# Kernel tuning notes

Hardware: AMD Instinct MI355X
Metric: run time of the kernel (lower is better)

The kernel has to match this reference:

```python
import jax, jax.numpy as jnp
from jax import lax
import numpy as np

DELTA = 2
KUP = 5


def setup_inputs() -> dict:
    key = jax.random.key(0)
    ks = jax.random.split(key, 7)
    N, C, H, W = 4, 256, 64, 64
    Cm, outC = 64, 256
    enc_out = DELTA ** 2 * KUP ** 2  # 100
    return {
        "x": jax.random.normal(ks[0], (N, C, H, W), dtype=jnp.float32),
        "W_down": jax.random.normal(ks[1], (Cm, C), dtype=jnp.float32) * (1.0 / np.sqrt(C)),
        "b_down": jax.random.normal(ks[2], (Cm,), dtype=jnp.float32) * 0.01,
        "W_enc": jax.random.normal(ks[3], (enc_out, Cm, 3, 3), dtype=jnp.float32) * (1.0 / np.sqrt(Cm * 9)),
        "b_enc": jax.random.normal(ks[4], (enc_out,), dtype=jnp.float32) * 0.01,
        "W_out": jax.random.normal(ks[5], (outC, C), dtype=jnp.float32) * (1.0 / np.sqrt(C)),
        "b_out": jax.random.normal(ks[6], (outC,), dtype=jnp.float32) * 0.01,
    }


def reference(x, W_down, b_down, W_enc, b_enc, W_out, b_out):
    N, C, H, W = x.shape
    d, Kup = DELTA, KUP
    K2, d2 = Kup * Kup, d * d

    # 1x1 down conv (Cm channels)
    t = jnp.einsum('nchw,mc->nmhw', x, W_down) + b_down[None, :, None, None]
    # 3x3 encoder conv -> (N, K2*d2, H, W); channel layout (k, i, j) as in torch pixel_shuffle
    e = lax.conv_general_dilated(t, W_enc, (1, 1), 'SAME',
                                 dimension_numbers=('NCHW', 'OIHW', 'NCHW'))
    e = e + b_enc[None, :, None, None]
    e = e.reshape(N, K2, d, d, H, W)
    # softmax over the Kup^2 reassembly weights at each upsampled position
    kern = jax.nn.softmax(e, axis=1)
    # fold back: (N, H, W, K2, d2) -- last axis indexes sub-pixel (i*d + j)
    kern = kern.transpose(0, 4, 5, 1, 2, 3).reshape(N, H, W, K2, d2)

    # unfold padded input into Kup x Kup neighborhoods: (N, C, H, W, K2)
    p = Kup // 2
    xp = jnp.pad(x, ((0, 0), (0, 0), (p, p), (p, p)))
    patches = jnp.stack([xp[:, :, i:i + H, j:j + W]
                         for i in range(Kup) for j in range(Kup)], axis=-1)

    # content-aware reassembly: (N, H, W, C, d2)
    out = jnp.einsum('nchwk,nhwkp->nhwcp', patches, kern)
    # pixel shuffle to (N, C, H*d, W*d)
    out = out.reshape(N, H, W, C, d, d).transpose(0, 3, 1, 4, 2, 5).reshape(N, C, H * d, W * d)
    # final 1x1 conv
    out = jnp.einsum('nchw,oc->nohw', out, W_out) + b_out[None, :, None, None]
    return out
```

## Files before the change

kernel.cpp:

```cpp
#include <hip/hip_runtime.h>

constexpr int N_  = 4;
constexpr int C_  = 256;
constexpr int H_  = 64;
constexpr int W_  = 64;
constexpr int Cm_ = 64;
constexpr int ENC = 100;
constexpr int OC_ = 256;
constexpr int HW_ = H_ * W_;
constexpr int H2_ = 128, W2_ = 128;

typedef float  f32x16 __attribute__((ext_vector_type(16)));
typedef float  f32x4  __attribute__((ext_vector_type(4)));
typedef float  f32x2  __attribute__((ext_vector_type(2)));
typedef short  s16x8  __attribute__((ext_vector_type(8)));

__device__ inline unsigned short f2bf(float f) {
    unsigned int u = __float_as_uint(f);
    unsigned int r = u + 0x7FFFu + ((u >> 16) & 1u);
    return (unsigned short)(r >> 16);
}
__device__ inline unsigned int cvt_pk_bf16(float a, float b) {
    unsigned int r;
    asm volatile("v_cvt_pk_bf16_f32 %0, %1, %2" : "=v"(r) : "v"(a), "v"(b));
    return r;
}
__device__ inline f32x2 bfp2f(unsigned int u) {
    f32x2 r;
    r.x = __uint_as_float(u << 16);
    r.y = __uint_as_float(u & 0xffff0000u);
    return r;
}
__device__ inline void pk_fma_lo(f32x2& d, f32x2 a, f32x2 b) {
    asm volatile("v_pk_fma_f32 %0, %1, %2, %0 op_sel:[0,0,0] op_sel_hi:[1,0,1]"
                 : "+v"(d) : "v"(a), "v"(b));
}
__device__ inline void pk_fma_hi(f32x2& d, f32x2 a, f32x2 b) {
    asm volatile("v_pk_fma_f32 %0, %1, %2, %0 op_sel:[0,1,0] op_sel_hi:[1,1,1]"
                 : "+v"(d) : "v"(a), "v"(b));
}

__global__ __launch_bounds__(256) void k_prep(const float* __restrict__ Wo,
                                              const float* __restrict__ Wd,
                                              const float* __restrict__ We,
                                              unsigned short* __restrict__ Wcat,
                                              unsigned short* __restrict__ Web) {
    int bb  = blockIdx.x;
    int tid = threadIdx.x;
    if (bb < 320) {
        int idx = bb * 256 + tid;
        int row = idx >> 8, c = idx & 255;
        float v = (row < 256) ? Wo[idx] : Wd[(row - 256) * 256 + c];
        Wcat[idx] = f2bf(v);
    } else {
        int idx = (bb - 320) * 256 + tid;
        int tap = idx >> 13;
        int rem = idx & 8191;
        int o   = rem >> 6;
        int m   = rem & 63;
        Web[idx] = (o < ENC) ? f2bf(We[(o * Cm_ + m) * 9 + tap]) : (unsigned short)0;
    }
}

__global__ __launch_bounds__(640) void k_gemm(const float* __restrict__ x,
                                              const unsigned short* __restrict__ Wcat,
                                              const float* __restrict__ bd,
                                              unsigned short* __restrict__ y1b,
                                              unsigned short* __restrict__ t2) {
    int b   = blockIdx.x;
    int wh  = b & 1;
    int h   = (b >> 1) & 63;
    int n   = b >> 7;
    int tid  = threadIdx.x;
    int lane = tid & 63;
    int wv   = tid >> 6;

    __shared__ unsigned short xs[32 * 260];

    {
        unsigned int* xd = (unsigned int*)xs;
        for (int idx = tid; idx < 1024; idx += 640) {
            int c2  = idx >> 3;
            int pg4 = idx & 7;
            const float* xc = x + (size_t)n * C_ * HW_ + (size_t)(c2 * 2) * HW_
                                + h * 64 + wh * 32 + pg4 * 4;
            float4 a  = *(const float4*)xc;
            float4 bq = *(const float4*)(xc + HW_);
            int base = (pg4 * 4) * 130 + c2;
            xd[base]       = cvt_pk_bf16(a.x, bq.x);
            xd[base + 130] = cvt_pk_bf16(a.y, bq.y);
            xd[base + 260] = cvt_pk_bf16(a.z, bq.z);
            xd[base + 390] = cvt_pk_bf16(a.w, bq.w);
        }
    }
    __syncthreads();

    f32x16 acc;
#pragma unroll
    for (int i = 0; i < 16; i++) acc[i] = 0.f;

    int oL   = lane & 31;
    int half = lane >> 5;
    const unsigned short* wb = Wcat + ((size_t)(wv * 32 + oL)) * C_ + half * 8;
    const unsigned short* tb = &xs[(lane & 31) * 260 + half * 8];

    s16x8 wf[2];
    *(uint4*)&wf[0] = *(const uint4*)&wb[0];
    for (int kc = 0; kc < 16; kc++) {
        int cur = kc & 1;
        if (kc < 15)
            *(uint4*)&wf[cur ^ 1] = *(const uint4*)&wb[(kc + 1) * 16];
        s16x8 bfv;
        ((uint2*)&bfv)[0] = *(const uint2*)&tb[kc * 16];
        ((uint2*)&bfv)[1] = *(const uint2*)&tb[kc * 16 + 4];
        acc = __builtin_amdgcn_mfma_f32_32x32x16_bf16(wf[cur], bfv, acc, 0, 0, 0);
    }

    int col = lane & 31;
    int pix = h * 64 + wh * 32 + col;
    if (wv < 8) {
#pragma unroll
        for (int r = 0; r < 16; r++) {
            int o = wv * 32 + (r & 3) + 8 * (r >> 2) + 4 * half;
            y1b[((size_t)(n * OC_ + o)) * HW_ + pix] = f2bf(acc[r]);
        }
    } else {
        unsigned short* tp = t2 + ((size_t)(n * HW_ + pix)) * 64;
#pragma unroll
        for (int r = 0; r < 16; r += 2) {
            int m = (wv - 8) * 32 + (r & 3) + 8 * (r >> 2) + 4 * half;
            float2 bdv = *(const float2*)&bd[m];
            *(unsigned int*)&tp[m] = cvt_pk_bf16(acc[r] + bdv.x, acc[r + 1] + bdv.y);
        }
    }
}

__global__ __launch_bounds__(256) void k_encsm(const unsigned short* __restrict__ t2,
                                               const unsigned short* __restrict__ Web,
                                               const float* __restrict__ be,
                                               float* __restrict__ kern2) {
    int b    = blockIdx.x;
    int ph   = b & 1;
    int h    = (b >> 1) & 63;
    int n    = b >> 7;
    int pix0 = ph * 32;
    int tid  = threadIdx.x;
    int lane = tid & 63;
    int wv   = tid >> 6;
    int o0   = wv * 32;

    __shared__ unsigned short ts[3 * 34 * 68];
    __shared__ float          es[32 * 105];

    for (int idx = tid; idx < 3 * 34 * 8; idx += 256) {
        int r   = idx / 272;
        int rem = idx - r * 272;
        int cw  = rem >> 3;
        int mc  = rem & 7;
        int gh  = h - 1 + r;
        int gw  = pix0 + cw - 1;
        uint2 lo = make_uint2(0u, 0u), hi = make_uint2(0u, 0u);
        if (gh >= 0 && gh < H_ && gw >= 0 && gw < W_) {
            uint4 v = *(const uint4*)&t2[((size_t)(n * HW_ + gh * W_ + gw)) * 64 + mc * 8];
            lo = make_uint2(v.x, v.y); hi = make_uint2(v.z, v.w);
        }
        int la = (r * 34 + cw) * 68 + mc * 8;
        *(uint2*)&ts[la]     = lo;
        *(uint2*)&ts[la + 4] = hi;
    }
    __syncthreads();

    f32x16 acc;
#pragma unroll
    for (int i = 0; i < 16; i++) acc[i] = 0.f;

    int oL   = lane & 31;
    int half = lane >> 5;
    const unsigned short* wb = Web + ((size_t)(o0 + oL)) * 64 + half * 8;

    s16x8 wf[2][4];
#pragma unroll
    for (int kc = 0; kc < 4; kc++)
        *(uint4*)&wf[0][kc] = *(const uint4*)&wb[kc * 16];

    for (int tap = 0; tap < 9; tap++) {
        int cur = tap & 1;
        if (tap < 8) {
            const unsigned short* wn = wb + (size_t)(tap + 1) * 128 * 64;
#pragma unroll
            for (int kc = 0; kc < 4; kc++)
                *(uint4*)&wf[cur ^ 1][kc] = *(const uint4*)&wn[kc * 16];
        }
        int di = tap / 3, dj = tap % 3;
        int cw = (lane & 31) + dj;
        const unsigned short* tb = &ts[(di * 34 + cw) * 68 + half * 8];
#pragma unroll
        for (int kc = 0; kc < 4; kc++) {
            s16x8 bfv;
            ((uint2*)&bfv)[0] = *(const uint2*)&tb[kc * 16];
            ((uint2*)&bfv)[1] = *(const uint2*)&tb[kc * 16 + 4];
            acc = __builtin_amdgcn_mfma_f32_32x32x16_bf16(wf[cur][kc], bfv, acc, 0, 0, 0);
        }
    }

    int pixl = lane & 31;
#pragma unroll
    for (int r = 0; r < 16; r++) {
        int o = o0 + (r & 3) + 8 * (r >> 2) + 4 * half;
        if (o < ENC)
            es[pixl * 105 + o] = acc[r] + be[o];
    }
    __syncthreads();

    if (tid < 128) {
        int pix = tid & 31;
        int ij  = tid >> 5;
        float v[25];
        float mx = -1e30f;
#pragma unroll
        for (int k = 0; k < 25; k++) {
            v[k] = es[pix * 105 + k * 4 + ij];
            mx   = fmaxf(mx, v[k]);
        }
        float s = 0.f;
#pragma unroll
        for (int k = 0; k < 25; k++) {
            v[k] = __expf(v[k] - mx);
            s += v[k];
        }
        float inv = 1.0f / s;
        float* kp = kern2 + (size_t)(n * 64 + h) * 6400 + (size_t)(pix0 + pix) * 4 + ij;
#pragma unroll
        for (int k = 0; k < 25; k++) kp[k * 256] = v[k] * inv;
    }
}

__global__ __launch_bounds__(256) void k_reasm(const unsigned short* __restrict__ y1b,
                                               const float* __restrict__ kern2,
                                               const float* __restrict__ bo,
                                               float* __restrict__ out) {
    int b  = blockIdx.x;
    int og = b & 7;
    int h  = (b >> 3) & 63;
    int n  = b >> 9;
    int o0 = og * 32;
    int tid = threadIdx.x;
    int wp  = tid & 31;
    int ol  = tid >> 5;

    __shared__ float ks[25 * 256 + 8];

    {
        const float4* src = (const float4*)(kern2 + (size_t)(n * 64 + h) * 6400);
        float4* dst = (float4*)ks;
#pragma unroll
        for (int i = 0; i < 7; i++) {
            int idx = tid + i * 256;
            if (idx < 1600) {
                int k = idx >> 6, j = idx & 63;
                dst[(k << 6) + (j ^ ((j >> 3) & 1))] = src[idx];
            }
        }
    }

    unsigned int yraw[4][5][3];
    {
        const unsigned short* yb = y1b + ((size_t)(n * OC_ + o0 + ol * 4)) * HW_ + (2 * wp - 2);
#pragma unroll
        for (int o = 0; o < 4; o++) {
#pragma unroll
            for (int di = 0; di < 5; di++) {
                int gh  = h - 2 + di;
                int ghc = gh < 0 ? 0 : (gh > H_ - 1 ? H_ - 1 : gh);
                bool rok = (gh >= 0) && (gh < H_);
                const unsigned short* yr = yb + (size_t)o * HW_ + ghc * W_;
                yraw[o][di][0] = (rok && wp > 0)  ? *(const unsigned int*)(yr)     : 0u;
                yraw[o][di][1] =  rok             ? *(const unsigned int*)(yr + 2) : 0u;
                yraw[o][di][2] = (rok && wp < 31) ? *(const unsigned int*)(yr + 4) : 0u;
            }
        }
    }
    __syncthreads();

    f32x2 acc[4][2][2];
#pragma unroll
    for (int o = 0; o < 4; o++)
#pragma unroll
        for (int w = 0; w < 2; w++)
#pragma unroll
            for (int p = 0; p < 2; p++) acc[o][w][p] = (f32x2)(0.f);

    const char* kb  = (const char*)ks + wp * 32;
    const int   fsw = (wp >> 2) & 1;
#pragma unroll
    for (int di = 0; di < 5; di++) {
        f32x2 yv[4][3];
#pragma unroll
        for (int o = 0; o < 4; o++)
#pragma unroll
            for (int q = 0; q < 3; q++)
                yv[o][q] = bfp2f(yraw[o][di][q]);
#pragma unroll
        for (int dj = 0; dj < 5; dj++) {
            const int k = di * 5 + dj;
            union { f32x4 v; f32x2 h2[2]; } kw0, kw1;
            kw0.v = *(const f32x4*)(kb + k * 1024 + (fsw << 4));
            kw1.v = *(const f32x4*)(kb + k * 1024 + 16 - (fsw << 4));
#pragma unroll
            for (int o = 0; o < 4; o++) {
                f32x2 pa = yv[o][dj >> 1];
                f32x2 pb = yv[o][(dj + 1) >> 1];
                if (dj & 1) {
                    pk_fma_hi(acc[o][0][0], kw0.h2[0], pa);
                    pk_fma_hi(acc[o][0][1], kw0.h2[1], pa);
                    pk_fma_lo(acc[o][1][0], kw1.h2[0], pb);
                    pk_fma_lo(acc[o][1][1], kw1.h2[1], pb);
                } else {
                    pk_fma_lo(acc[o][0][0], kw0.h2[0], pa);
                    pk_fma_lo(acc[o][0][1], kw0.h2[1], pa);
                    pk_fma_hi(acc[o][1][0], kw1.h2[0], pb);
                    pk_fma_hi(acc[o][1][1], kw1.h2[1], pb);
                }
            }
        }
    }

#pragma unroll
    for (int o = 0; o < 4; o++) {
        int oo = o0 + ol * 4 + o;
        float bias = bo[oo];
        float* op = out + (((size_t)(n * OC_ + oo)) * H2_ + 2 * h) * W2_ + 4 * wp;
        float4 r0 = make_float4(acc[o][0][0].x + bias, acc[o][0][0].y + bias,
                                acc[o][1][0].x + bias, acc[o][1][0].y + bias);
        float4 r1 = make_float4(acc[o][0][1].x + bias, acc[o][0][1].y + bias,
                                acc[o][1][1].x + bias, acc[o][1][1].y + bias);
        *(float4*)op         = r0;
        *(float4*)(op + W2_) = r1;
    }
}

extern "C" void kernel_launch(void* const* d_in, const int* in_sizes, int n_in,
                              void* d_out, int out_size, void* d_ws, size_t ws_size,
                              hipStream_t stream) {
    const float* x  = (const float*)d_in[0];
    const float* Wd = (const float*)d_in[1];
    const float* bd = (const float*)d_in[2];
    const float* We = (const float*)d_in[3];
    const float* be = (const float*)d_in[4];
    const float* Wo = (const float*)d_in[5];
    const float* bo = (const float*)d_in[6];
    float* out = (float*)d_out;

    char* wsb = (char*)d_ws;
    unsigned short* y1b  = (unsigned short*)wsb;
    float*          kern2= (float*)(wsb + 8388608);
    unsigned short* Wcat = (unsigned short*)(wsb + 8388608);
    unsigned short* t2   = (unsigned short*)(wsb + 14942208);
    unsigned short* Web  = (unsigned short*)(wsb + 17039360);

    k_prep  <<<608,  256, 0, stream>>>(Wo, Wd, We, Wcat, Web);
    k_gemm  <<<512,  640, 0, stream>>>(x, Wcat, bd, y1b, t2);
    k_encsm <<<512,  256, 0, stream>>>(t2, Web, be, kern2);
    k_reasm <<<2048, 256, 0, stream>>>(y1b, kern2, bo, out);
}
```

Measured before the change: 139.9 us.

## Stage t2 writes through LDS, split encoder accumulators, reorder reassembly blocks

```diff
diff --git a/kernel.cpp b/kernel.cpp
--- a/kernel.cpp
+++ b/kernel.cpp
@@ -76,6 +76,7 @@
     int wv   = tid >> 6;
 
     __shared__ unsigned short xs[32 * 260];
+    __shared__ unsigned short tbuf[32 * 72];
 
     {
         unsigned int* xd = (unsigned int*)xs;
@@ -118,6 +119,17 @@
 
     int col = lane & 31;
     int pix = h * 64 + wh * 32 + col;
+
+    if (wv >= 8) {
+#pragma unroll
+        for (int r = 0; r < 16; r += 2) {
+            int m = (wv - 8) * 32 + (r & 3) + 8 * (r >> 2) + 4 * half;
+            float2 bdv = *(const float2*)&bd[m];
+            *(unsigned int*)&tbuf[col * 72 + m] = cvt_pk_bf16(acc[r] + bdv.x, acc[r + 1] + bdv.y);
+        }
+    }
+    __syncthreads();
+
     if (wv < 8) {
 #pragma unroll
         for (int r = 0; r < 16; r++) {
@@ -125,13 +137,15 @@
             y1b[((size_t)(n * OC_ + o)) * HW_ + pix] = f2bf(acc[r]);
         }
     } else {
-        unsigned short* tp = t2 + ((size_t)(n * HW_ + pix)) * 64;
-#pragma unroll
-        for (int r = 0; r < 16; r += 2) {
-            int m = (wv - 8) * 32 + (r & 3) + 8 * (r >> 2) + 4 * half;
-            float2 bdv = *(const float2*)&bd[m];
-            *(unsigned int*)&tp[m] = cvt_pk_bf16(acc[r] + bdv.x, acc[r + 1] + bdv.y);
-        }
+        int idx = tid - 512;
+        int row = idx >> 2;
+        int p   = idx & 3;
+        const uint4* src = (const uint4*)&tbuf[row * 72 + p * 16];
+        uint4 v0 = src[0];
+        uint4 v1 = src[1];
+        uint4* dst = (uint4*)(t2 + ((size_t)(n * HW_ + h * 64 + wh * 32 + row)) * 64 + p * 16);
+        dst[0] = v0;
+        dst[1] = v1;
     }
 }
 
@@ -170,9 +184,9 @@
     }
     __syncthreads();
 
-    f32x16 acc;
-#pragma unroll
-    for (int i = 0; i < 16; i++) acc[i] = 0.f;
+    f32x16 acc0, acc1;
+#pragma unroll
+    for (int i = 0; i < 16; i++) { acc0[i] = 0.f; acc1[i] = 0.f; }
 
     int oL   = lane & 31;
     int half = lane >> 5;
@@ -199,16 +213,21 @@
             s16x8 bfv;
             ((uint2*)&bfv)[0] = *(const uint2*)&tb[kc * 16];
             ((uint2*)&bfv)[1] = *(const uint2*)&tb[kc * 16 + 4];
-            acc = __builtin_amdgcn_mfma_f32_32x32x16_bf16(wf[cur][kc], bfv, acc, 0, 0, 0);
-        }
-    }
+            if (kc & 1)
+                acc1 = __builtin_amdgcn_mfma_f32_32x32x16_bf16(wf[cur][kc], bfv, acc1, 0, 0, 0);
+            else
+                acc0 = __builtin_amdgcn_mfma_f32_32x32x16_bf16(wf[cur][kc], bfv, acc0, 0, 0, 0);
+        }
+    }
+#pragma unroll
+    for (int i = 0; i < 16; i++) acc0[i] += acc1[i];
 
     int pixl = lane & 31;
 #pragma unroll
     for (int r = 0; r < 16; r++) {
         int o = o0 + (r & 3) + 8 * (r >> 2) + 4 * half;
         if (o < ENC)
-            es[pixl * 105 + o] = acc[r] + be[o];
+            es[pixl * 105 + o] = acc0[r] + be[o];
     }
     __syncthreads();
 
@@ -240,8 +259,8 @@
                                                const float* __restrict__ bo,
                                                float* __restrict__ out) {
     int b  = blockIdx.x;
-    int og = b & 7;
-    int h  = (b >> 3) & 63;
+    int h  = b & 63;
+    int og = (b >> 6) & 7;
     int n  = b >> 9;
     int o0 = og * 32;
     int tid = threadIdx.x;
```

New measurement: 135.9 us, median of 2. -2.9%, faster.
